# Performance work log

Measured on AMD Instinct MI355X. Metric: run time of the kernel, lower is better.

Reference implementation:

```python
import jax, jax.numpy as jnp
import numpy as np

HIDDEN = 2048
NUM_HEADS = 16
HEAD_DIM = HIDDEN // NUM_HEADS  # 128
ROPE_BASE = 10000.0
BATCH = 2
SEQ = 2048


def _rope_cos_sin(seq_len, dim, base):
    inv_freq = 1.0 / (base ** (jnp.arange(0, dim, 2, dtype=jnp.float32) / dim))
    t = jnp.arange(seq_len, dtype=jnp.float32)
    freqs = jnp.outer(t, inv_freq)              # [S, dim/2]
    emb = jnp.concatenate([freqs, freqs], -1)   # [S, dim]
    return jnp.cos(emb), jnp.sin(emb)


def _rotate_half(x):
    d = x.shape[-1] // 2
    return jnp.concatenate([-x[..., d:], x[..., :d]], axis=-1)


def setup_inputs() -> dict:
    key = jax.random.key(0)
    ks = jax.random.split(key, 5)
    s = 1.0 / np.sqrt(HIDDEN)
    return {
        "hidden_states": jax.random.normal(ks[0], (BATCH, SEQ, HIDDEN), jnp.float32),
        "wq": jax.random.normal(ks[1], (HIDDEN, HIDDEN), jnp.float32) * s,
        "wk": jax.random.normal(ks[2], (HIDDEN, HIDDEN), jnp.float32) * s,
        "wv": jax.random.normal(ks[3], (HIDDEN, HIDDEN), jnp.float32) * s,
        "wo": jax.random.normal(ks[4], (HIDDEN, HIDDEN), jnp.float32) * s,
    }


def reference(hidden_states, wq, wk, wv, wo):
    b, s, _ = hidden_states.shape
    # Linear(bias=False): y = x @ W.T
    def proj(x, w):
        y = jnp.einsum('bsh,dh->bsd', x, w)
        return y.reshape(b, s, NUM_HEADS, HEAD_DIM).transpose(0, 2, 1, 3)  # [B,H,S,D]

    q = proj(hidden_states, wq)
    k = proj(hidden_states, wk)
    v = proj(hidden_states, wv)

    cos, sin = _rope_cos_sin(s, HEAD_DIM, ROPE_BASE)  # [S, D], broadcasts over B,H
    q = q * cos + _rotate_half(q) * sin
    k = k * cos + _rotate_half(k) * sin

    scale = 1.0 / np.sqrt(HEAD_DIM)
    scores = jnp.einsum('bhqd,bhkd->bhqk', q, k) * scale          # [B,H,S,S]
    attn = jax.nn.softmax(scores.astype(jnp.float32), axis=-1).astype(q.dtype)
    out = jnp.einsum('bhqk,bhkd->bhqd', attn, v)                  # [B,H,S,D]
    out = out.transpose(0, 2, 1, 3).reshape(b, s, HIDDEN)
    return jnp.einsum('bsh,dh->bsd', out, wo)
```

## Files before the change

kernel.cpp:

```cpp
#include <hip/hip_runtime.h>
#include <cstdint>
#include <cstddef>

typedef unsigned short u16;
typedef __attribute__((ext_vector_type(8))) __bf16 bf16x8;
typedef __attribute__((ext_vector_type(4))) float f32x4;
typedef __attribute__((ext_vector_type(8))) u16 u16x8;

#define GAS __attribute__((address_space(1)))
#define LAS __attribute__((address_space(3)))

static __device__ __forceinline__ u16 f2bf(float f) {
  uint32_t u = __builtin_bit_cast(uint32_t, f);
  u += 0x7fffu + ((u >> 16) & 1u);
  return (u16)(u >> 16);
}
static __device__ __forceinline__ float bf2f(u16 v) {
  uint32_t u = ((uint32_t)v) << 16;
  return __builtin_bit_cast(float, u);
}
static __device__ __forceinline__ bf16x8 ldf(const u16* p) {
  return __builtin_bit_cast(bf16x8, *reinterpret_cast<const u16x8*>(p));
}
static __device__ __forceinline__ void gld16(const void* g, void* l) {
  __builtin_amdgcn_global_load_lds((GAS unsigned int*)(uintptr_t)g,
                                   (LAS unsigned int*)l, 16, 0, 0);
}
#define MFMA __builtin_amdgcn_mfma_f32_16x16x32_bf16

__global__ __launch_bounds__(256) void castk(const float* __restrict__ s,
                                             u16* __restrict__ d, int n4) {
  int i = blockIdx.x * 256 + threadIdx.x;
  if (i < n4) {
    const float4 v = reinterpret_cast<const float4*>(s)[i];
    ushort4 o;
    o.x = f2bf(v.x); o.y = f2bf(v.y); o.z = f2bf(v.z); o.w = f2bf(v.w);
    reinterpret_cast<ushort4*>(d)[i] = o;
  }
}

__global__ __launch_bounds__(512, 2)
void gemm256(const u16* __restrict__ A, const u16* __restrict__ B,
             void* __restrict__ Cp, int M, int N, int K, int out_f32, int nbx) {
  __shared__ alignas(16) u16 sm[8][8192];
  const int tid = threadIdx.x;
  const int lane = tid & 63, w = tid >> 6;
  const int wm = w >> 2, wn = w & 3;
  const int lo = lane & 15, hi8 = (lane >> 4) << 3;

  const int nwg = gridDim.x;
  const int id = blockIdx.x;
  const int idp = (id & 7) * (nwg >> 3) + (id >> 3);
  const long m0 = (long)(idp / nbx) * 256;
  const long n0 = (long)(idp % nbx) * 256;

  const int srow = w * 16 + (lane >> 2);
  const int scol = (lane & 3) * 8;
  const u16* pA0 = A + (size_t)(m0 + srow) * K + scol;
  const u16* pA1 = A + (size_t)(m0 + 128 + srow) * K + scol;
  const u16* pB0 = B + (size_t)(n0 + srow) * K + scol;
  const u16* pB1 = B + (size_t)(n0 + 128 + srow) * K + scol;
  const int ldso = w * 512;

  auto stA = [&](int slot, int half, int k0) {
    u16* d = sm[(slot << 2) | half];
    gld16(pA0 + k0 + half * 32, d + ldso);
    gld16(pA1 + k0 + half * 32, d + 4096 + ldso);
  };
  auto stB = [&](int slot, int half, int k0) {
    u16* d = sm[(slot << 2) | 2 | half];
    gld16(pB0 + k0 + half * 32, d + ldso);
    gld16(pB1 + k0 + half * 32, d + 4096 + ldso);
  };

  const int aoff = (wm * 128 + lo) * 32 + hi8;
  const int boff = (wn * 64 + lo) * 32 + hi8;

  f32x4 acc[8][4] = {};

  stA(0, 0, 0); stB(0, 0, 0); stA(0, 1, 0); stB(0, 1, 0);
  asm volatile("s_waitcnt vmcnt(4)" ::: "memory");
  __builtin_amdgcn_s_barrier();

  const int NT = K >> 6;
  for (int kt = 0; kt < NT; ++kt) {
    const int s = kt & 1, so = s ^ 1;
    const int kn = (kt + 1 < NT) ? ((kt + 1) << 6) : 0;
    const u16* sA0 = sm[(s << 2) | 0];
    const u16* sA1 = sm[(s << 2) | 1];
    const u16* sB0 = sm[(s << 2) | 2];
    const u16* sB1 = sm[(s << 2) | 3];

    bf16x8 af[8], b0, b1;
    b0 = ldf(sB0 + boff);
    b1 = ldf(sB0 + boff + 512);
#pragma unroll
    for (int mf = 0; mf < 8; ++mf) af[mf] = ldf(sA0 + aoff + mf * 512);
    stA(so, 0, kn);
    __builtin_amdgcn_s_barrier();
    asm volatile("s_waitcnt lgkmcnt(0)" ::: "memory");
    __builtin_amdgcn_s_setprio(1);
#pragma unroll
    for (int mf = 0; mf < 8; ++mf) {
      acc[mf][0] = MFMA(af[mf], b0, acc[mf][0], 0, 0, 0);
      acc[mf][1] = MFMA(af[mf], b1, acc[mf][1], 0, 0, 0);
    }
    __builtin_amdgcn_s_setprio(0);
    __builtin_amdgcn_s_barrier();
    b0 = ldf(sB0 + boff + 1024);
    b1 = ldf(sB0 + boff + 1536);
    stB(so, 0, kn);
    __builtin_amdgcn_s_barrier();
    asm volatile("s_waitcnt lgkmcnt(0)" ::: "memory");
    __builtin_amdgcn_s_setprio(1);
#pragma unroll
    for (int mf = 0; mf < 8; ++mf) {
      acc[mf][2] = MFMA(af[mf], b0, acc[mf][2], 0, 0, 0);
      acc[mf][3] = MFMA(af[mf], b1, acc[mf][3], 0, 0, 0);
    }
    __builtin_amdgcn_s_setprio(0);
    asm volatile("s_waitcnt vmcnt(4)" ::: "memory");
    __builtin_amdgcn_s_barrier();
    b0 = ldf(sB1 + boff);
    b1 = ldf(sB1 + boff + 512);
#pragma unroll
    for (int mf = 0; mf < 8; ++mf) af[mf] = ldf(sA1 + aoff + mf * 512);
    stA(so, 1, kn);
    __builtin_amdgcn_s_barrier();
    asm volatile("s_waitcnt lgkmcnt(0)" ::: "memory");
    __builtin_amdgcn_s_setprio(1);
#pragma unroll
    for (int mf = 0; mf < 8; ++mf) {
      acc[mf][0] = MFMA(af[mf], b0, acc[mf][0], 0, 0, 0);
      acc[mf][1] = MFMA(af[mf], b1, acc[mf][1], 0, 0, 0);
    }
    __builtin_amdgcn_s_setprio(0);
    __builtin_amdgcn_s_barrier();
    b0 = ldf(sB1 + boff + 1024);
    b1 = ldf(sB1 + boff + 1536);
    stB(so, 1, kn);
    __builtin_amdgcn_s_barrier();
    asm volatile("s_waitcnt lgkmcnt(0)" ::: "memory");
    __builtin_amdgcn_s_setprio(1);
#pragma unroll
    for (int mf = 0; mf < 8; ++mf) {
      acc[mf][2] = MFMA(af[mf], b0, acc[mf][2], 0, 0, 0);
      acc[mf][3] = MFMA(af[mf], b1, acc[mf][3], 0, 0, 0);
    }
    __builtin_amdgcn_s_setprio(0);
    asm volatile("s_waitcnt vmcnt(4)" ::: "memory");
    __builtin_amdgcn_s_barrier();
  }
  asm volatile("s_waitcnt vmcnt(0)" ::: "memory");

#pragma unroll
  for (int mf = 0; mf < 8; ++mf)
#pragma unroll
    for (int nf = 0; nf < 4; ++nf) {
      const long row = m0 + wm * 128 + mf * 16 + (lane >> 4) * 4;
      const long col = n0 + wn * 64 + nf * 16 + lo;
      if (out_f32) {
        float* C = (float*)Cp;
#pragma unroll
        for (int r = 0; r < 4; ++r) C[(row + r) * N + col] = acc[mf][nf][r];
      } else {
        u16* C = (u16*)Cp;
#pragma unroll
        for (int r = 0; r < 4; ++r) C[(row + r) * N + col] = f2bf(acc[mf][nf][r]);
      }
    }
}

__global__ __launch_bounds__(256) void rope_q(u16* __restrict__ QKV) {
  const int m = blockIdx.x;
  const int pos = m & 2047;
  const int t = threadIdx.x;
  const int j = t & 63;
  const float invf = exp2f(-(float)j * 0.20762050593046014f);
  float sn, cs;
  sincosf((float)pos * invf, &sn, &cs);
  const float sc = 0.08838834764831845f;
#pragma unroll
  for (int h = t >> 6; h < 16; h += 4) {
    u16* p = QKV + (size_t)m * 6144 + h * 128;
    float a = bf2f(p[j]), b = bf2f(p[j + 64]);
    p[j]      = f2bf((a * cs - b * sn) * sc);
    p[j + 64] = f2bf((b * cs + a * sn) * sc);
  }
}

__global__ __launch_bounds__(256) void rope_k(const u16* __restrict__ QKV, u16* __restrict__ Kb) {
  const int m = blockIdx.x;
  const int pos = m & 2047;
  const int bb = m >> 11;
  const int kb = pos >> 6;
  const int key = pos & 63;
  const int t = threadIdx.x;
  const int j = t & 63;
  const float invf = exp2f(-(float)j * 0.20762050593046014f);
  float sn, cs;
  sincosf((float)pos * invf, &sn, &cs);
  const int sw = (key & 7) << 3;
#pragma unroll
  for (int h = t >> 6; h < 16; h += 4) {
    const u16* p = QKV + (size_t)m * 6144 + 2048 + h * 128;
    float a = bf2f(p[j]), b = bf2f(p[j + 64]);
    u16* dst = Kb + ((size_t)(bb * 16 + h) * 32 + kb) * 8192 + key * 128;
    dst[j ^ sw]        = f2bf(a * cs - b * sn);
    dst[(j + 64) ^ sw] = f2bf(b * cs + a * sn);
  }
}

__global__ __launch_bounds__(256) void transpose_v(const u16* __restrict__ QKV, u16* __restrict__ Vb) {
  __shared__ u16 smv[64][130];
  const int kb = blockIdx.x, bh = blockIdx.y;
  const int bb = bh >> 4, h = bh & 15;
  const int t = threadIdx.x;
#pragma unroll
  for (int r = 0; r < 4; ++r) {
    int c = r * 256 + t;
    int key = c >> 4, d0 = (c & 15) * 8;
    const u16* src = QKV + (size_t)(bb * 2048 + kb * 64 + key) * 6144 + 4096 + h * 128 + d0;
    u16x8 v = *reinterpret_cast<const u16x8*>(src);
#pragma unroll
    for (int i = 0; i < 8; ++i) smv[key][d0 + i] = v[i];
  }
  __syncthreads();
  u16* dst = Vb + ((size_t)bh * 32 + kb) * 8192;
#pragma unroll
  for (int r = 0; r < 4; ++r) {
    int c = r * 256 + t;
    int key0 = (c & 7) * 8, d = c >> 3;
    u16x8 v;
#pragma unroll
    for (int i = 0; i < 8; ++i) v[i] = smv[key0 + i][d];
    *reinterpret_cast<u16x8*>(dst + d * 64 + (key0 ^ ((d & 7) << 3))) = v;
  }
}

__global__ __launch_bounds__(256, 2)
void flash_attn(const u16* __restrict__ Q, const u16* __restrict__ Kb,
                const u16* __restrict__ Vb, u16* __restrict__ O) {
  __shared__ alignas(16) u16 smK[64 * 128];
  __shared__ alignas(16) u16 smV[128 * 64];
  __shared__ alignas(16) u16 smP[4][16 * 64];

  const int f = blockIdx.x;
  const int bh = (f & 7) * 4 + (f >> 8);
  const int qb = (f >> 3) & 31;
  const int bb = bh >> 4, h = bh & 15;
  const int lane = threadIdx.x & 63, w = threadIdx.x >> 6;

  const int qrow = bb * 2048 + qb * 64 + w * 16 + (lane & 15);
  const u16* qp = Q + (size_t)qrow * 6144 + h * 128 + ((lane >> 4) * 8);
  bf16x8 qf[4];
#pragma unroll
  for (int kk = 0; kk < 4; ++kk) qf[kk] = ldf(qp + kk * 32);

  f32x4 oacc[8] = {};
  float mr[4] = {-__builtin_inff(), -__builtin_inff(), -__builtin_inff(), -__builtin_inff()};
  float lr[4] = {0.f, 0.f, 0.f, 0.f};

  const u16* kbase = Kb + (size_t)bh * 32 * 8192;
  const u16* vbase = Vb + (size_t)bh * 32 * 8192;

  for (int kb = 0; kb < 32; ++kb) {
    __syncthreads();
#pragma unroll
    for (int j = 0; j < 4; ++j) {
      int off = (j * 4 + w) * 512;
      gld16(kbase + (size_t)kb * 8192 + off + lane * 8, &smK[off]);
      gld16(vbase + (size_t)kb * 8192 + off + lane * 8, &smV[off]);
    }
    __syncthreads();

    f32x4 sacc[4] = {};
    __builtin_amdgcn_s_setprio(1);
#pragma unroll
    for (int nt = 0; nt < 4; ++nt) {
      const int key = nt * 16 + (lane & 15);
      const int sw = (key & 7) << 3;
#pragma unroll
      for (int kk = 0; kk < 4; ++kk) {
        const int d = kk * 32 + (lane >> 4) * 8;
        bf16x8 kf = ldf(&smK[key * 128 + (d ^ sw)]);
        sacc[nt] = MFMA(qf[kk], kf, sacc[nt], 0, 0, 0);
      }
    }
    __builtin_amdgcn_s_setprio(0);

    float nm[4], fac[4];
#pragma unroll
    for (int r = 0; r < 4; ++r) {
      float mx = fmaxf(fmaxf(sacc[0][r], sacc[1][r]), fmaxf(sacc[2][r], sacc[3][r]));
#pragma unroll
      for (int o = 1; o < 16; o <<= 1) mx = fmaxf(mx, __shfl_xor(mx, o));
      nm[r] = fmaxf(mr[r], mx);
      fac[r] = exp2f((mr[r] - nm[r]) * 1.4426950408889634f);
      mr[r] = nm[r];
    }
#pragma unroll
    for (int nt = 0; nt < 4; ++nt)
#pragma unroll
      for (int r = 0; r < 4; ++r)
        sacc[nt][r] = exp2f((sacc[nt][r] - nm[r]) * 1.4426950408889634f);
#pragma unroll
    for (int r = 0; r < 4; ++r) {
      float s = (sacc[0][r] + sacc[1][r]) + (sacc[2][r] + sacc[3][r]);
#pragma unroll
      for (int o = 1; o < 16; o <<= 1) s += __shfl_xor(s, o);
      lr[r] = lr[r] * fac[r] + s;
    }
#pragma unroll
    for (int t = 0; t < 8; ++t)
#pragma unroll
      for (int r = 0; r < 4; ++r) oacc[t][r] *= fac[r];

    u16* pw = smP[w];
#pragma unroll
    for (int r = 0; r < 4; ++r) {
      const int row = (lane >> 4) * 4 + r;
      const int sw = (row & 7) << 3;
#pragma unroll
      for (int nt = 0; nt < 4; ++nt) {
        const int col = nt * 16 + (lane & 15);
        pw[row * 64 + (col ^ sw)] = f2bf(sacc[nt][r]);
      }
    }

    __builtin_amdgcn_s_setprio(1);
#pragma unroll
    for (int kk2 = 0; kk2 < 2; ++kk2) {
      const int k0 = kk2 * 32 + (lane >> 4) * 8;
      const int prow = lane & 15;
      bf16x8 pf = ldf(&pw[prow * 64 + (k0 ^ ((prow & 7) << 3))]);
#pragma unroll
      for (int t = 0; t < 8; ++t) {
        const int d = t * 16 + (lane & 15);
        bf16x8 vf = ldf(&smV[d * 64 + (k0 ^ ((d & 7) << 3))]);
        oacc[t] = MFMA(pf, vf, oacc[t], 0, 0, 0);
      }
    }
    __builtin_amdgcn_s_setprio(0);
  }

#pragma unroll
  for (int r = 0; r < 4; ++r) lr[r] = 1.0f / lr[r];
  const int orow0 = bb * 2048 + qb * 64 + w * 16;
#pragma unroll
  for (int t = 0; t < 8; ++t)
#pragma unroll
    for (int r = 0; r < 4; ++r) {
      const int row = orow0 + (lane >> 4) * 4 + r;
      const int d = t * 16 + (lane & 15);
      O[(size_t)row * 2048 + h * 128 + d] = f2bf(oacc[t][r] * lr[r]);
    }
}

extern "C" void kernel_launch(void* const* d_in, const int* in_sizes, int n_in,
                              void* d_out, int out_size, void* d_ws, size_t ws_size,
                              hipStream_t stream) {
  const float* X  = (const float*)d_in[0];
  const float* Wq = (const float*)d_in[1];
  const float* Wk = (const float*)d_in[2];
  const float* Wv = (const float*)d_in[3];
  const float* Wo = (const float*)d_in[4];
  float* out = (float*)d_out;
  char* ws = (char*)d_ws;
  const size_t MB = 1u << 20;
  u16* Xb    = (u16*)(ws + 0 * MB);
  u16* QKVb  = (u16*)(ws + 16 * MB);
  u16* Wqkvb = (u16*)(ws + 64 * MB);
  u16* Wob   = (u16*)(ws + 96 * MB);
  u16* Kblk  = Xb;
  u16* Vblk  = (u16*)(ws + 64 * MB);
  u16* Ob    = (u16*)(ws + 80 * MB);

  castk<<<8192, 256, 0, stream>>>(X,  Xb, 2097152);
  castk<<<4096, 256, 0, stream>>>(Wq, Wqkvb, 1048576);
  castk<<<4096, 256, 0, stream>>>(Wk, Wqkvb + 4194304, 1048576);
  castk<<<4096, 256, 0, stream>>>(Wv, Wqkvb + 8388608, 1048576);
  castk<<<4096, 256, 0, stream>>>(Wo, Wob, 1048576);

  gemm256<<<384, 512, 0, stream>>>(Xb, Wqkvb, QKVb, 4096, 6144, 2048, 0, 24);

  rope_q<<<4096, 256, 0, stream>>>(QKVb);
  rope_k<<<4096, 256, 0, stream>>>(QKVb, Kblk);
  transpose_v<<<dim3(32, 32), 256, 0, stream>>>(QKVb, Vblk);

  flash_attn<<<1024, 256, 0, stream>>>(QKVb, Kblk, Vblk, Ob);

  gemm256<<<128, 512, 0, stream>>>(Ob, Wob, out, 4096, 2048, 2048, 1, 8);
}
```

Before: 499.7 us.

## Rewrite flash attention with 32x32 MFMA, 128-row Q tiles and lazy rescaling

Replaces the flash attention kernel with a version that uses 32x32x16 bf16 MFMAs, computes S transposed so each lane owns one query row, and processes 128 query rows per block (32 per wave), halving the grid. The log2(e) factor moves into the Q RoPE scale so exp2 needs no multiply, and the output/denominator rescale is skipped unless the running max grows by more than 8 in log2 space. This is meant to cut cross-lane shuffles for the softmax reductions and reuse each K/V tile across twice as many queries. In exchange it raises register pressure (launch bounds ask for 3 blocks per SM) and the lazy rescale lets the exponentials grow by up to a factor of 256 before renormalising.

```diff
diff --git a/kernel.cpp b/kernel.cpp
--- a/kernel.cpp
+++ b/kernel.cpp
@@ -5,6 +5,7 @@
 typedef unsigned short u16;
 typedef __attribute__((ext_vector_type(8))) __bf16 bf16x8;
 typedef __attribute__((ext_vector_type(4))) float f32x4;
+typedef __attribute__((ext_vector_type(16))) float f32x16;
 typedef __attribute__((ext_vector_type(8))) u16 u16x8;
 
 #define GAS __attribute__((address_space(1)))
@@ -27,6 +28,7 @@
                                    (LAS unsigned int*)l, 16, 0, 0);
 }
 #define MFMA __builtin_amdgcn_mfma_f32_16x16x32_bf16
+#define MFMA32 __builtin_amdgcn_mfma_f32_32x32x16_bf16
 
 __global__ __launch_bounds__(256) void castk(const float* __restrict__ s,
                                              u16* __restrict__ d, int n4) {
@@ -179,7 +181,7 @@
   const float invf = exp2f(-(float)j * 0.20762050593046014f);
   float sn, cs;
   sincosf((float)pos * invf, &sn, &cs);
-  const float sc = 0.08838834764831845f;
+  const float sc = 0.08838834764831845f * 1.4426950408889634f;
 #pragma unroll
   for (int h = t >> 6; h < 16; h += 4) {
     u16* p = QKV + (size_t)m * 6144 + h * 128;
@@ -238,123 +240,134 @@
   }
 }
 
-__global__ __launch_bounds__(256, 2)
-void flash_attn(const u16* __restrict__ Q, const u16* __restrict__ Kb,
-                const u16* __restrict__ Vb, u16* __restrict__ O) {
-  __shared__ alignas(16) u16 smK[64 * 128];
-  __shared__ alignas(16) u16 smV[128 * 64];
-  __shared__ alignas(16) u16 smP[4][16 * 64];
-
-  const int f = blockIdx.x;
-  const int bh = (f & 7) * 4 + (f >> 8);
-  const int qb = (f >> 3) & 31;
+__global__ __launch_bounds__(256, 3)
+void flash3(const u16* __restrict__ Q, const u16* __restrict__ Kb,
+            const u16* __restrict__ Vb, u16* __restrict__ O) {
+  __shared__ alignas(16) u16 smK[8192];
+  __shared__ alignas(16) u16 smV[8192];
+  __shared__ alignas(16) u16 smP[4][2048];
+
+  const int id = blockIdx.x;
+  const int bh = id & 31, qb = id >> 5;
   const int bb = bh >> 4, h = bh & 15;
-  const int lane = threadIdx.x & 63, w = threadIdx.x >> 6;
-
-  const int qrow = bb * 2048 + qb * 64 + w * 16 + (lane & 15);
-  const u16* qp = Q + (size_t)qrow * 6144 + h * 128 + ((lane >> 4) * 8);
-  bf16x8 qf[4];
-#pragma unroll
-  for (int kk = 0; kk < 4; ++kk) qf[kk] = ldf(qp + kk * 32);
-
-  f32x4 oacc[8] = {};
-  float mr[4] = {-__builtin_inff(), -__builtin_inff(), -__builtin_inff(), -__builtin_inff()};
-  float lr[4] = {0.f, 0.f, 0.f, 0.f};
+  const int tid = threadIdx.x, lane = tid & 63, w = tid >> 6;
+  const int q5 = lane & 31, hi = lane >> 5;
+
+  const int qrow = bb * 2048 + qb * 128 + w * 32 + q5;
+  const u16* qp = Q + (size_t)qrow * 6144 + h * 128 + hi * 8;
+  bf16x8 qf[8];
+#pragma unroll
+  for (int ds = 0; ds < 8; ++ds) qf[ds] = ldf(qp + ds * 16);
 
   const u16* kbase = Kb + (size_t)bh * 32 * 8192;
   const u16* vbase = Vb + (size_t)bh * 32 * 8192;
 
-  for (int kb = 0; kb < 32; ++kb) {
+  f32x16 oacc[4] = {};
+  float mr = -__builtin_inff(), lr = 0.f;
+
+  const int k0row = q5 * 128, k1row = (32 + q5) * 128;
+  const int ksw = (q5 & 7) << 3;
+  const int dh = hi * 8;
+  u16* pwarp = smP[w];
+
+  for (int kt = 0; kt < 32; ++kt) {
     __syncthreads();
+    const u16* ks = kbase + (size_t)kt * 8192;
+    const u16* vs = vbase + (size_t)kt * 8192;
 #pragma unroll
     for (int j = 0; j < 4; ++j) {
-      int off = (j * 4 + w) * 512;
-      gld16(kbase + (size_t)kb * 8192 + off + lane * 8, &smK[off]);
-      gld16(vbase + (size_t)kb * 8192 + off + lane * 8, &smV[off]);
+      const int off = (w * 4 + j) * 512;
+      gld16(ks + off + lane * 8, &smK[off]);
+      gld16(vs + off + lane * 8, &smV[off]);
     }
     __syncthreads();
 
-    f32x4 sacc[4] = {};
-    __builtin_amdgcn_s_setprio(1);
-#pragma unroll
-    for (int nt = 0; nt < 4; ++nt) {
-      const int key = nt * 16 + (lane & 15);
-      const int sw = (key & 7) << 3;
-#pragma unroll
-      for (int kk = 0; kk < 4; ++kk) {
-        const int d = kk * 32 + (lane >> 4) * 8;
-        bf16x8 kf = ldf(&smK[key * 128 + (d ^ sw)]);
-        sacc[nt] = MFMA(qf[kk], kf, sacc[nt], 0, 0, 0);
+    f32x16 s0 = {}, s1 = {};
+    __builtin_amdgcn_s_setprio(1);
+#pragma unroll
+    for (int ds = 0; ds < 8; ++ds) {
+      const int dd = (ds * 16 + dh) ^ ksw;
+      bf16x8 kf0 = ldf(&smK[k0row + dd]);
+      bf16x8 kf1 = ldf(&smK[k1row + dd]);
+      s0 = MFMA32(kf0, qf[ds], s0, 0, 0, 0);
+      s1 = MFMA32(kf1, qf[ds], s1, 0, 0, 0);
+    }
+    __builtin_amdgcn_s_setprio(0);
+
+    float v[32];
+#pragma unroll
+    for (int i = 0; i < 16; ++i) { v[i] = s0[i]; v[16 + i] = s1[i]; }
+#pragma unroll
+    for (int st = 16; st >= 1; st >>= 1)
+#pragma unroll
+      for (int i = 0; i < st; ++i) v[i] = fmaxf(v[i], v[i + st]);
+    float pm = fmaxf(v[0], __shfl_xor(v[0], 32));
+
+    if (!__all(pm - mr <= 8.0f)) {
+      float nm = fmaxf(mr, pm);
+      float fac = exp2f(mr - nm);
+      lr *= fac;
+#pragma unroll
+      for (int db = 0; db < 4; ++db)
+#pragma unroll
+        for (int i = 0; i < 16; ++i) oacc[db][i] *= fac;
+      mr = nm;
+    }
+
+#pragma unroll
+    for (int i = 0; i < 16; ++i) {
+      s0[i] = exp2f(s0[i] - mr);
+      s1[i] = exp2f(s1[i] - mr);
+    }
+#pragma unroll
+    for (int i = 0; i < 16; ++i) { v[i] = s0[i]; v[16 + i] = s1[i]; }
+#pragma unroll
+    for (int st = 16; st >= 1; st >>= 1)
+#pragma unroll
+      for (int i = 0; i < st; ++i) v[i] += v[i + st];
+    lr += v[0] + __shfl_xor(v[0], 32);
+
+#pragma unroll
+    for (int i = 0; i < 8; ++i) {
+      const int r = 2 * i;
+      const int key0 = (r & 3) + 8 * (r >> 2) + 4 * hi;
+      const uint32_t p0 = (uint32_t)f2bf(s0[r]) | ((uint32_t)f2bf(s0[r + 1]) << 16);
+      const uint32_t p1 = (uint32_t)f2bf(s1[r]) | ((uint32_t)f2bf(s1[r + 1]) << 16);
+      *reinterpret_cast<uint32_t*>(&pwarp[q5 * 64 + (key0 ^ ksw)]) = p0;
+      *reinterpret_cast<uint32_t*>(&pwarp[q5 * 64 + ((key0 + 32) ^ ksw)]) = p1;
+    }
+
+    bf16x8 pa[4];
+#pragma unroll
+    for (int ks2 = 0; ks2 < 4; ++ks2)
+      pa[ks2] = ldf(&pwarp[q5 * 64 + ((ks2 * 16 + dh) ^ ksw)]);
+
+    __builtin_amdgcn_s_setprio(1);
+#pragma unroll
+    for (int db = 0; db < 4; ++db) {
+      const int d = db * 32 + q5;
+      const int vrow = d * 64;
+      const int vsw = (d & 7) << 3;
+#pragma unroll
+      for (int ks2 = 0; ks2 < 4; ++ks2) {
+        bf16x8 vf = ldf(&smV[vrow + ((ks2 * 16 + dh) ^ vsw)]);
+        oacc[db] = MFMA32(pa[ks2], vf, oacc[db], 0, 0, 0);
       }
     }
     __builtin_amdgcn_s_setprio(0);
-
-    float nm[4], fac[4];
-#pragma unroll
-    for (int r = 0; r < 4; ++r) {
-      float mx = fmaxf(fmaxf(sacc[0][r], sacc[1][r]), fmaxf(sacc[2][r], sacc[3][r]));
-#pragma unroll
-      for (int o = 1; o < 16; o <<= 1) mx = fmaxf(mx, __shfl_xor(mx, o));
-      nm[r] = fmaxf(mr[r], mx);
-      fac[r] = exp2f((mr[r] - nm[r]) * 1.4426950408889634f);
-      mr[r] = nm[r];
-    }
-#pragma unroll
-    for (int nt = 0; nt < 4; ++nt)
-#pragma unroll
-      for (int r = 0; r < 4; ++r)
-        sacc[nt][r] = exp2f((sacc[nt][r] - nm[r]) * 1.4426950408889634f);
-#pragma unroll
-    for (int r = 0; r < 4; ++r) {
-      float s = (sacc[0][r] + sacc[1][r]) + (sacc[2][r] + sacc[3][r]);
-#pragma unroll
-      for (int o = 1; o < 16; o <<= 1) s += __shfl_xor(s, o);
-      lr[r] = lr[r] * fac[r] + s;
-    }
-#pragma unroll
-    for (int t = 0; t < 8; ++t)
-#pragma unroll
-      for (int r = 0; r < 4; ++r) oacc[t][r] *= fac[r];
-
-    u16* pw = smP[w];
-#pragma unroll
-    for (int r = 0; r < 4; ++r) {
-      const int row = (lane >> 4) * 4 + r;
-      const int sw = (row & 7) << 3;
-#pragma unroll
-      for (int nt = 0; nt < 4; ++nt) {
-        const int col = nt * 16 + (lane & 15);
-        pw[row * 64 + (col ^ sw)] = f2bf(sacc[nt][r]);
-      }
-    }
-
-    __builtin_amdgcn_s_setprio(1);
-#pragma unroll
-    for (int kk2 = 0; kk2 < 2; ++kk2) {
-      const int k0 = kk2 * 32 + (lane >> 4) * 8;
-      const int prow = lane & 15;
-      bf16x8 pf = ldf(&pw[prow * 64 + (k0 ^ ((prow & 7) << 3))]);
-#pragma unroll
-      for (int t = 0; t < 8; ++t) {
-        const int d = t * 16 + (lane & 15);
-        bf16x8 vf = ldf(&smV[d * 64 + (k0 ^ ((d & 7) << 3))]);
-        oacc[t] = MFMA(pf, vf, oacc[t], 0, 0, 0);
-      }
-    }
-    __builtin_amdgcn_s_setprio(0);
-  }
-
-#pragma unroll
-  for (int r = 0; r < 4; ++r) lr[r] = 1.0f / lr[r];
-  const int orow0 = bb * 2048 + qb * 64 + w * 16;
-#pragma unroll
-  for (int t = 0; t < 8; ++t)
-#pragma unroll
-    for (int r = 0; r < 4; ++r) {
-      const int row = orow0 + (lane >> 4) * 4 + r;
-      const int d = t * 16 + (lane & 15);
-      O[(size_t)row * 2048 + h * 128 + d] = f2bf(oacc[t][r] * lr[r]);
-    }
+  }
+
+  const float rinv = 1.0f / lr;
+  const int qgb = bb * 2048 + qb * 128 + w * 32;
+  const int colb = h * 128 + q5;
+#pragma unroll
+  for (int reg = 0; reg < 16; ++reg) {
+    const int qq = (reg & 3) + 8 * (reg >> 2) + 4 * hi;
+    const float rv = __shfl(rinv, qq);
+#pragma unroll
+    for (int db = 0; db < 4; ++db)
+      O[(size_t)(qgb + qq) * 2048 + db * 32 + colb] = f2bf(oacc[db][reg] * rv);
+  }
 }
 
 extern "C" void kernel_launch(void* const* d_in, const int* in_sizes, int n_in,
@@ -388,7 +401,7 @@
   rope_k<<<4096, 256, 0, stream>>>(QKVb, Kblk);
   transpose_v<<<dim3(32, 32), 256, 0, stream>>>(QKVb, Vblk);
 
-  flash_attn<<<1024, 256, 0, stream>>>(QKVb, Kblk, Vblk, Ob);
+  flash3<<<512, 256, 0, stream>>>(QKVb, Kblk, Vblk, Ob);
 
   gemm256<<<128, 512, 0, stream>>>(Ob, Wob, out, 4096, 2048, 2048, 1, 8);
 }
```

After: 493.1 us. No clear change (-1.3%).
